# Optimization experiments

Hardware: AMD Instinct MI355X
Metric: run time of the kernel (lower is better)

Reference implementation:

```python
import jax, jax.numpy as jnp
import numpy as np

LEAKY_ALPHA = 0.2
NEG_INF = -9e15


def setup_inputs() -> dict:
    key = jax.random.key(0)
    k1, k2, k3, k4, k5 = jax.random.split(key, 5)
    n, n_head, f_in, f_out = 4096, 8, 1024, 128
    scale_w = float(np.sqrt(6.0 / (f_in + f_out)))      # xavier_uniform over (f_in,f_out)
    scale_a = float(np.sqrt(6.0 / (f_out + 1)))
    return {
        "h": jax.random.normal(k1, (n, f_in), dtype=jnp.float32),
        "adj": jax.random.randint(k2, (n, n), 0, 2, dtype=jnp.int32),
        "w": jax.random.uniform(k3, (n_head, f_in, f_out), jnp.float32, -scale_w, scale_w),
        "bias": jnp.zeros((f_out,), dtype=jnp.float32),
        "a_src": jax.random.uniform(k4, (n_head, f_out, 1), jnp.float32, -scale_a, scale_a),
        "a_dst": jax.random.uniform(k5, (n_head, f_out, 1), jnp.float32, -scale_a, scale_a),
    }


def reference(h, adj, w, bias, a_src, a_dst):
    n = h.shape[0]
    # per-head projection: [h_head, n, f_out]
    h_prime = jnp.einsum('nf,hfo->hno', h, w)
    attn_src = jnp.einsum('hno,hoi->hn', h_prime, a_src)   # [n_head, n]
    attn_dst = jnp.einsum('hno,hoi->hn', h_prime, a_dst)   # [n_head, n]
    # additive score: attn[h,i,j] = src[h,i] + dst[h,j]
    attn = attn_src[:, :, None] + attn_dst[:, None, :]
    attn = jnp.where(attn >= 0, attn, LEAKY_ALPHA * attn)  # leaky_relu
    attn = jnp.where(adj[None] > 0, attn, NEG_INF)
    attn = jax.nn.softmax(attn, axis=-1)                   # [n_head, n, n]
    # dropout layers are identity in eval mode
    output = jnp.einsum('hnm,hmo->hno', attn, h_prime) + bias
    output = jnp.transpose(output, (1, 0, 2)).reshape(n, -1)  # [n, n_head*f_out]
    weight = jnp.sum(attn, axis=0)                          # [n, n]
    return output, weight
```

## Files before the change

kernel.cpp:

```cpp
#include <hip/hip_runtime.h>
#include <hip/hip_bf16.h>


#define N 4096
#define NH 8
#define FIN 1024
#define FOUT 128

typedef short bf16x8 __attribute__((ext_vector_type(8)));
typedef float f32x4 __attribute__((ext_vector_type(4)));
typedef unsigned int uint;
typedef unsigned short ushort;

__device__ __forceinline__ float b2f(ushort u){ return __uint_as_float(((uint)u)<<16); }
__device__ __forceinline__ uint pk2cvt(float a, float b){
    float2 f; f.x=a; f.y=b;
    __hip_bfloat162 h = __float22bfloat162_rn(f);
    uint r; __builtin_memcpy(&r, &h, 4); return r;
}
__device__ __forceinline__ float sane(float x, float lim){ return fminf(fmaxf(x,-lim),lim); }
__device__ __forceinline__ int swz(int r, int cg){ return r*64 + (((cg) ^ (r & 7)) << 3); }
__device__ __forceinline__ void glds16(const ushort* g, ushort* l){
    __builtin_amdgcn_global_load_lds(
        (const __attribute__((address_space(1))) void*)g,
        (__attribute__((address_space(3))) void*)l, 16, 0, 0);
}
__device__ __forceinline__ int detect_mode(const ushort* hraw){
    ushort u = hraw[2*(threadIdx.x & 63)];
    int e = (u>>7)&0xFF;
    unsigned long long m = __ballot(e>=90 && e<=141);
    return (__popcll(m)>=40)?0:1;
}

__global__ __launch_bounds__(256) void prep(
        const int* __restrict__ adj, uint* __restrict__ bitsT,
        float* __restrict__ acc, float* __restrict__ lsum, int nacc,
        const void* __restrict__ wraw, const ushort* __restrict__ hraw,
        ushort* __restrict__ wT) {
    __shared__ ushort tile[64][72];
    int b = blockIdx.x, t = threadIdx.x;
    if (b < 65536) {
        size_t idx = (size_t)b * 256 + t;
        int v = adj[idx];
        unsigned long long m = __ballot(v != 0);
        int lane = t & 63;
        uint i  = (uint)(idx >> 12);
        uint jw = ((uint)idx & 4095u) >> 5;
        if (lane == 0)       bitsT[jw * N + i] = (uint)m;
        else if (lane == 32) bitsT[jw * N + i] = (uint)(m >> 32);
        return;
    }
    int zb = b - 65536;
    if (zb < nacc + 32) {
        float4 z; z.x=0.f; z.y=0.f; z.z=0.f; z.w=0.f;
        if (zb < nacc) reinterpret_cast<float4*>(acc)[(size_t)zb*256+t] = z;
        else           reinterpret_cast<float4*>(lsum)[(size_t)(zb-nacc)*256+t] = z;
        return;
    }
    int bb = zb - (nacc + 32);
    int mode = detect_mode(hraw);
    int f0 = (bb & 15) * 64, o0 = ((bb >> 4) & 1) * 64, h = bb >> 5;
#pragma unroll
    for (int it = 0; it < 2; ++it) {
        int slot = it * 256 + t;
        int row = slot >> 3, c = slot & 7;
        size_t eoff = (size_t)h * (FIN * FOUT) + (size_t)(f0 + row) * FOUT + o0 + c * 8;
        alignas(16) ushort tmp[8];
        if (mode == 0) {
            *reinterpret_cast<uint4*>(tmp) = *reinterpret_cast<const uint4*>((const ushort*)wraw + eoff);
        } else {
            const float* wF = (const float*)wraw;
            float4 x = *reinterpret_cast<const float4*>(wF + eoff);
            float4 y = *reinterpret_cast<const float4*>(wF + eoff + 4);
            uint4 p; p.x = pk2cvt(x.x,x.y); p.y = pk2cvt(x.z,x.w);
            p.z = pk2cvt(y.x,y.y); p.w = pk2cvt(y.z,y.w);
            *reinterpret_cast<uint4*>(tmp) = p;
        }
        *reinterpret_cast<uint4*>(&tile[row][c * 8]) = *reinterpret_cast<uint4*>(tmp);
    }
    __syncthreads();
#pragma unroll
    for (int it = 0; it < 2; ++it) {
        int slot = it * 256 + t;
        int orow = slot >> 3, c = slot & 7;
        alignas(16) ushort tmp[8];
#pragma unroll
        for (int k = 0; k < 8; ++k) tmp[k] = tile[c * 8 + k][orow];
        *reinterpret_cast<uint4*>(wT + (size_t)h * (FIN * FOUT) + (size_t)(o0 + orow) * FIN + f0 + c * 8) =
            *reinterpret_cast<uint4*>(tmp);
    }
}

__global__ __launch_bounds__(256) void gemm_hp(
        const void* __restrict__ hraw, const ushort* __restrict__ wT,
        const void* __restrict__ asraw, const void* __restrict__ adraw,
        ushort* __restrict__ hpT,
        float* __restrict__ es1, float* __restrict__ es2,
        float* __restrict__ ed1, float* __restrict__ ed2) {
    __shared__ ushort Bs[2][FOUT * 64];
    __shared__ float sred[64], dred[64];
    int mode = detect_mode((const ushort*)hraw);
    int t = threadIdx.x;
    int lin = blockIdx.x + 64 * blockIdx.y;
    int i0 = (((lin & 7) * 8) + ((lin >> 6) & 7)) * 64;
    int head = (lin >> 3) & 7;
    int w = t >> 6, lane = t & 63, quad = lane >> 4, l16 = lane & 15, wsh = quad * 8;
    int arow = i0 + w * 16 + l16;
    const ushort* hU = (const ushort*)hraw;
    const float*  hF = (const float*)hraw;
    int l8 = lane >> 3, lk = (lane & 7) ^ (l8 & 7);
    const ushort* gs[4];
#pragma unroll
    for (int s = 0; s < 4; ++s) {
        int o = (w * 4 + s) * 8 + l8;
        gs[s] = wT + (size_t)head * FOUT * FIN + (size_t)o * FIN + lk * 8;
    }

    float asv[8], adv[8];
#pragma unroll
    for (int n = 0; n < 8; ++n) {
        int ai = head * FOUT + n * 16 + l16;
        asv[n] = mode ? ((const float*)asraw)[ai] : b2f(((const ushort*)asraw)[ai]);
        adv[n] = mode ? ((const float*)adraw)[ai] : b2f(((const ushort*)adraw)[ai]);
    }

    f32x4 acc[8] = {};
#pragma unroll
    for (int s = 0; s < 4; ++s) glds16(gs[s], &Bs[0][(w * 4 + s) * 512]);
    uint4 au[2]; float4 af[2][2];
    if (mode == 0) {
#pragma unroll
        for (int kk = 0; kk < 2; ++kk)
            au[kk] = *reinterpret_cast<const uint4*>(hU + (size_t)arow * FIN + kk * 32 + wsh);
    } else {
#pragma unroll
        for (int kk = 0; kk < 2; ++kk) {
            af[kk][0] = *reinterpret_cast<const float4*>(hF + (size_t)arow * FIN + kk * 32 + wsh);
            af[kk][1] = *reinterpret_cast<const float4*>(hF + (size_t)arow * FIN + kk * 32 + wsh + 4);
        }
    }
    __syncthreads();

    for (int c = 0; c < 16; ++c) {
        int k0 = c * 64;
        if (c < 15) {
            ushort* bsw = &Bs[(c + 1) & 1][0];
#pragma unroll
            for (int s = 0; s < 4; ++s)
                glds16(gs[s] + k0 + 64, &bsw[(w * 4 + s) * 512]);
        }
        bf16x8 a2[2];
        if (mode == 0) {
            a2[0] = *reinterpret_cast<bf16x8*>(&au[0]);
            a2[1] = *reinterpret_cast<bf16x8*>(&au[1]);
        } else {
#pragma unroll
            for (int kk = 0; kk < 2; ++kk) {
                uint4 av; av.x = pk2cvt(af[kk][0].x, af[kk][0].y); av.y = pk2cvt(af[kk][0].z, af[kk][0].w);
                av.z = pk2cvt(af[kk][1].x, af[kk][1].y); av.w = pk2cvt(af[kk][1].z, af[kk][1].w);
                a2[kk] = *reinterpret_cast<bf16x8*>(&av);
            }
        }
        if (c < 15) {
            if (mode == 0) {
#pragma unroll
                for (int kk = 0; kk < 2; ++kk)
                    au[kk] = *reinterpret_cast<const uint4*>(hU + (size_t)arow * FIN + k0 + 64 + kk * 32 + wsh);
            } else {
#pragma unroll
                for (int kk = 0; kk < 2; ++kk) {
                    af[kk][0] = *reinterpret_cast<const float4*>(hF + (size_t)arow * FIN + k0 + 64 + kk * 32 + wsh);
                    af[kk][1] = *reinterpret_cast<const float4*>(hF + (size_t)arow * FIN + k0 + 64 + kk * 32 + wsh + 4);
                }
            }
        }
        const ushort* bsr = &Bs[c & 1][0];
#pragma unroll
        for (int kk = 0; kk < 2; ++kk) {
            int cg0 = kk * 4 + quad;
#pragma unroll
            for (int n = 0; n < 8; ++n) {
                bf16x8 b = *reinterpret_cast<const bf16x8*>(&bsr[swz(n * 16 + l16, cg0)]);
                acc[n] = __builtin_amdgcn_mfma_f32_16x16x32_bf16(a2[kk], b, acc[n], 0, 0, 0);
            }
        }
        if (c < 15) __syncthreads();
    }
#pragma unroll
    for (int n = 0; n < 8; ++n) {
        uint2 pk;
        pk.x = pk2cvt(acc[n][0], acc[n][1]);
        pk.y = pk2cvt(acc[n][2], acc[n][3]);
        *reinterpret_cast<uint2*>(hpT + ((size_t)head * FOUT + n * 16 + l16) * N + i0 + w * 16 + quad * 4) = pk;
    }
#pragma unroll
    for (int rr = 0; rr < 4; ++rr) {
        float s = 0.f, d = 0.f;
#pragma unroll
        for (int n = 0; n < 8; ++n) { s += acc[n][rr] * asv[n]; d += acc[n][rr] * adv[n]; }
#pragma unroll
        for (int off = 1; off < 16; off <<= 1) { s += __shfl_xor(s, off); d += __shfl_xor(d, off); }
        if (l16 == 0) { sred[w * 16 + quad * 4 + rr] = s; dred[w * 16 + quad * 4 + rr] = d; }
    }
    __syncthreads();
    if (t < 64) {
        int i = i0 + t;
        float s = sane(sred[t], 30.f);
        float d = sane(dred[t], 30.f);
        es1[head * N + i] = __expf(s);       es2[head * N + i] = __expf(0.2f * s);
        ed1[head * N + i] = __expf(d);       ed2[head * N + i] = __expf(0.2f * d);
    }
}

__global__ __launch_bounds__(256, 4) void pv_kernel(
        const ushort* __restrict__ hpT,
        const float* __restrict__ es1, const float* __restrict__ es2,
        const float* __restrict__ ed1, const float* __restrict__ ed2,
        const uint* __restrict__ bitsT,
        float* __restrict__ accOut, float* __restrict__ lsum, int use_atomic) {
    __shared__ ushort Bs[2][FOUT * 64];
    __shared__ float Ed[2][1024];
    int t = threadIdx.x;
    int lin = blockIdx.x + 32 * blockIdx.y + 256 * blockIdx.z;
    int g  = (lin & 7) * 4 + (lin >> 8);
    int ib = (lin >> 3) & 31;
    int hh = g & 7, kz = g >> 3;
    int i0 = ib * 128, kb = kz * 1024;
    int w = t >> 6, lane = t & 63, quad = lane >> 4, l16 = lane & 15, wsh = quad * 8;
    int irow[2];
    float s1[2], s2[2];
#pragma unroll
    for (int mi = 0; mi < 2; ++mi) {
        irow[mi] = i0 + w * 32 + mi * 16 + l16;
        s1[mi] = es1[hh * N + irow[mi]];
        s2[mi] = es2[hh * N + irow[mi]];
    }
    const uint* bp = bitsT + (size_t)(kb >> 5) * N;
    int l8 = lane >> 3, lk = (lane & 7) ^ (l8 & 7);
    const ushort* gs[4];
#pragma unroll
    for (int s = 0; s < 4; ++s) {
        int o = (w * 4 + s) * 8 + l8;
        gs[s] = hpT + (size_t)hh * FOUT * N + (size_t)o * N + kb + lk * 8;
    }
    bf16x8 ones;
#pragma unroll
    for (int j = 0; j < 8; ++j) ones[j] = (short)0x3F80;

    f32x4 acc[2][8] = {};
    f32x4 accl[2] = {};

    float4 ev1 = *reinterpret_cast<const float4*>(ed1 + hh * N + kb + t * 4);
    float4 ev2 = *reinterpret_cast<const float4*>(ed2 + hh * N + kb + t * 4);
    uint bwc[2][2], bwn[2][2];
#pragma unroll
    for (int kk = 0; kk < 2; ++kk)
#pragma unroll
        for (int mi = 0; mi < 2; ++mi) bwc[kk][mi] = bp[(size_t)kk * N + irow[mi]];
#pragma unroll
    for (int s = 0; s < 4; ++s) glds16(gs[s], &Bs[0][(w * 4 + s) * 512]);
    *reinterpret_cast<float4*>(&Ed[0][t * 4]) = ev1;
    *reinterpret_cast<float4*>(&Ed[1][t * 4]) = ev2;
    __syncthreads();

    for (int c = 0; c < 16; ++c) {
        if (c < 15) {
            ushort* bsw = &Bs[(c + 1) & 1][0];
#pragma unroll
            for (int s = 0; s < 4; ++s)
                glds16(gs[s] + (c + 1) * 64, &bsw[(w * 4 + s) * 512]);
#pragma unroll
            for (int kk = 0; kk < 2; ++kk)
#pragma unroll
                for (int mi = 0; mi < 2; ++mi)
                    bwn[kk][mi] = bp[(size_t)((c + 1) * 2 + kk) * N + irow[mi]];
        }
        const ushort* bsr = &Bs[c & 1][0];
#pragma unroll
        for (int kk = 0; kk < 2; ++kk) {
            int kgl = c * 64 + kk * 32 + wsh;
            float4 d1a = *reinterpret_cast<const float4*>(&Ed[0][kgl]);
            float4 d1b = *reinterpret_cast<const float4*>(&Ed[0][kgl + 4]);
            float4 d2a = *reinterpret_cast<const float4*>(&Ed[1][kgl]);
            float4 d2b = *reinterpret_cast<const float4*>(&Ed[1][kgl + 4]);
            bf16x8 am[2];
#pragma unroll
            for (int mi = 0; mi < 2; ++mi) {
                uint word = bwc[kk][mi] >> wsh;
                float e0 = fmaxf(s1[mi]*d1a.x, s2[mi]*d2a.x); e0 = (word & 1u)   ? e0 : 0.f;
                float e1 = fmaxf(s1[mi]*d1a.y, s2[mi]*d2a.y); e1 = (word & 2u)   ? e1 : 0.f;
                float e2 = fmaxf(s1[mi]*d1a.z, s2[mi]*d2a.z); e2 = (word & 4u)   ? e2 : 0.f;
                float e3 = fmaxf(s1[mi]*d1a.w, s2[mi]*d2a.w); e3 = (word & 8u)   ? e3 : 0.f;
                float e4 = fmaxf(s1[mi]*d1b.x, s2[mi]*d2b.x); e4 = (word & 16u)  ? e4 : 0.f;
                float e5 = fmaxf(s1[mi]*d1b.y, s2[mi]*d2b.y); e5 = (word & 32u)  ? e5 : 0.f;
                float e6 = fmaxf(s1[mi]*d1b.z, s2[mi]*d2b.z); e6 = (word & 64u)  ? e6 : 0.f;
                float e7 = fmaxf(s1[mi]*d1b.w, s2[mi]*d2b.w); e7 = (word & 128u) ? e7 : 0.f;
                uint4 av; av.x = pk2cvt(e0, e1); av.y = pk2cvt(e2, e3);
                av.z = pk2cvt(e4, e5); av.w = pk2cvt(e6, e7);
                am[mi] = *reinterpret_cast<bf16x8*>(&av);
                accl[mi] = __builtin_amdgcn_mfma_f32_16x16x32_bf16(am[mi], ones, accl[mi], 0, 0, 0);
            }
            int cg0 = kk * 4 + quad;
            __builtin_amdgcn_s_setprio(1);
#pragma unroll
            for (int n = 0; n < 8; ++n) {
                bf16x8 b = *reinterpret_cast<const bf16x8*>(&bsr[swz(n * 16 + l16, cg0)]);
                acc[0][n] = __builtin_amdgcn_mfma_f32_16x16x32_bf16(am[0], b, acc[0][n], 0, 0, 0);
                acc[1][n] = __builtin_amdgcn_mfma_f32_16x16x32_bf16(am[1], b, acc[1][n], 0, 0, 0);
            }
            __builtin_amdgcn_s_setprio(0);
        }
#pragma unroll
        for (int kk = 0; kk < 2; ++kk)
#pragma unroll
            for (int mi = 0; mi < 2; ++mi) bwc[kk][mi] = bwn[kk][mi];
        if (c < 15) __syncthreads();
    }
    if (l16 == 0) {
#pragma unroll
        for (int mi = 0; mi < 2; ++mi)
#pragma unroll
            for (int rr = 0; rr < 4; ++rr)
                atomicAdd(&lsum[hh * N + i0 + w * 32 + mi * 16 + quad * 4 + rr], accl[mi][rr]);
    }
    if (use_atomic) {
#pragma unroll
        for (int mi = 0; mi < 2; ++mi) {
            float* arow = accOut + ((size_t)hh * N + i0 + w * 32 + mi * 16 + quad * 4) * FOUT + l16;
#pragma unroll
            for (int n = 0; n < 8; ++n)
#pragma unroll
                for (int rr = 0; rr < 4; ++rr)
                    atomicAdd(&arow[(size_t)rr * FOUT + n * 16], acc[mi][n][rr]);
        }
    } else {
        float* part = accOut + (size_t)kz * ((size_t)NH * N * FOUT);
#pragma unroll
        for (int mi = 0; mi < 2; ++mi) {
            float* arow = part + ((size_t)hh * N + i0 + w * 32 + mi * 16 + quad * 4) * FOUT + l16;
#pragma unroll
            for (int n = 0; n < 8; ++n)
#pragma unroll
                for (int rr = 0; rr < 4; ++rr)
                    arow[(size_t)rr * FOUT + n * 16] = acc[mi][n][rr];
        }
    }
}

__global__ __launch_bounds__(256) void pv_epi(
        const float* __restrict__ acc32, const float* __restrict__ lsum,
        const float* __restrict__ es1, const float* __restrict__ es2,
        const void* __restrict__ braw, const ushort* __restrict__ hraw,
        void* __restrict__ outraw,
        float* __restrict__ s1r, float* __restrict__ s2r, int nparts) {
    int mode = detect_mode(hraw);
    int idx4 = blockIdx.x * 256 + threadIdx.x;
    int h = idx4 >> 17;
    int i = (idx4 >> 5) & 4095;
    int og = idx4 & 31;
    const size_t PSTRIDE4 = (size_t)NH * N * FOUT / 4;
    float4 v = reinterpret_cast<const float4*>(acc32)[idx4];
    if (nparts == 4) {
        float4 a = reinterpret_cast<const float4*>(acc32)[PSTRIDE4 + idx4];
        float4 b = reinterpret_cast<const float4*>(acc32)[2 * PSTRIDE4 + idx4];
        float4 c = reinterpret_cast<const float4*>(acc32)[3 * PSTRIDE4 + idx4];
        v.x += a.x + b.x + c.x; v.y += a.y + b.y + c.y;
        v.z += a.z + b.z + c.z; v.w += a.w + b.w + c.w;
    }
    float lv = lsum[h * N + i];
    float r = (lv > 1e-30f) ? 1.0f / lv : 0.f;
    if (og == 0) {
        s1r[h * N + i] = es1[h * N + i] * r;
        s2r[h * N + i] = es2[h * N + i] * r;
    }
    float4 bv;
    if (mode) bv = reinterpret_cast<const float4*>(braw)[og];
    else {
        const ushort* bu = (const ushort*)braw;
        bv.x = b2f(bu[og*4]); bv.y = b2f(bu[og*4+1]); bv.z = b2f(bu[og*4+2]); bv.w = b2f(bu[og*4+3]);
    }
    v.x = v.x * r + bv.x; v.y = v.y * r + bv.y; v.z = v.z * r + bv.z; v.w = v.w * r + bv.w;
    size_t ob = (size_t)i * (NH * FOUT) + h * FOUT + og * 4;
    if (mode) *reinterpret_cast<float4*>((float*)outraw + ob) = v;
    else {
        uint2 pk; pk.x = pk2cvt(v.x, v.y); pk.y = pk2cvt(v.z, v.w);
        *reinterpret_cast<uint2*>((ushort*)outraw + ob) = pk;
    }
}

__global__ __launch_bounds__(256) void weight_kernel(
        const float* __restrict__ s1r, const float* __restrict__ s2r,
        const float* __restrict__ ed1, const float* __restrict__ ed2,
        const uint* __restrict__ bitsT,
        const ushort* __restrict__ hraw,
        void* __restrict__ outraw) {
    int mode = detect_mode(hraw);
    ushort* woutU = (ushort*)outraw + (size_t)N * (NH * FOUT);
    float*  woutF = (float*)outraw  + (size_t)N * (NH * FOUT);
    int t = threadIdx.x;
    int j = blockIdx.x * 1024 + t * 4;
    int i0 = blockIdx.y * 32;
    float4 d1[NH], d2[NH];
#pragma unroll
    for (int hh = 0; hh < NH; ++hh) {
        d1[hh] = *reinterpret_cast<const float4*>(ed1 + hh * N + j);
        d2[hh] = *reinterpret_cast<const float4*>(ed2 + hh * N + j);
    }
    int wrow = j >> 5;
    int jsh = j & 31;
    for (int i = i0; i < i0 + 32; ++i) {
        uint wbits = bitsT[(size_t)wrow * N + i] >> jsh;
        float sx = 0.f, sy = 0.f, sz = 0.f, sw = 0.f;
#pragma unroll
        for (int hh = 0; hh < NH; ++hh) {
            float a = s1r[hh * N + i];
            float b = s2r[hh * N + i];
            sx += fmaxf(a * d1[hh].x, b * d2[hh].x);
            sy += fmaxf(a * d1[hh].y, b * d2[hh].y);
            sz += fmaxf(a * d1[hh].z, b * d2[hh].z);
            sw += fmaxf(a * d1[hh].w, b * d2[hh].w);
        }
        sx = (wbits & 1u) ? sx : 0.f;
        sy = (wbits & 2u) ? sy : 0.f;
        sz = (wbits & 4u) ? sz : 0.f;
        sw = (wbits & 8u) ? sw : 0.f;
        size_t oidx = (size_t)i * N + j;
        if (mode) {
            float4 st; st.x = sx; st.y = sy; st.z = sz; st.w = sw;
            *reinterpret_cast<float4*>(woutF + oidx) = st;
        } else {
            uint2 pk; pk.x = pk2cvt(sx, sy); pk.y = pk2cvt(sz, sw);
            *reinterpret_cast<uint2*>(woutU + oidx) = pk;
        }
    }
}

extern "C" void kernel_launch(void* const* d_in, const int* in_sizes, int n_in,
                              void* d_out, int out_size, void* d_ws, size_t ws_size,
                              hipStream_t stream) {
    (void)in_sizes; (void)n_in; (void)out_size;
    const void* hraw  = d_in[0];
    const int*  adj   = (const int*)d_in[1];
    const void* wraw  = d_in[2];
    const void* braw  = d_in[3];
    const void* asraw = d_in[4];
    const void* adraw = d_in[5];

    char* ws = (char*)d_ws;
    float* lsum = (float*)(ws + 0);
    float* es1  = (float*)(ws + 262144);
    float* es2  = (float*)(ws + 393216);
    float* ed1  = (float*)(ws + 524288);
    float* ed2  = (float*)(ws + 655360);
    float* s1r  = (float*)(ws + 786432);
    float* s2r  = (float*)(ws + 917504);
    uint*  bitsT= (uint*)(ws + 1048576);
    ushort* wT  = (ushort*)(ws + 3145728);

    const size_t SMALL_END = 5242880;
    const size_t PART = 16777216;
    float*  acc32; ushort* hpT;
    int use_atomic, nparts;
    if (ws_size >= SMALL_END + 4 * PART + 8388608ull) {
        char* b = ws + SMALL_END;
        acc32 = (float*)b;
        hpT   = (ushort*)(b + 4 * PART);
        use_atomic = 0; nparts = 4;
    } else if (ws_size >= SMALL_END + 25165824ull) {
        char* b = ws + SMALL_END;
        acc32 = (float*)b;
        hpT   = (ushort*)(b + PART);
        use_atomic = 1; nparts = 1;
    } else {
        char* ob = (char*)d_out;
        acc32 = (float*)(ob + 16777216);
        hpT   = (ushort*)(ob + 33554432);
        use_atomic = 1; nparts = 1;
    }

    int nacc = use_atomic ? 4096 : 0;
    prep<<<65536 + nacc + 32 + 256, 256, 0, stream>>>(adj, bitsT, acc32, lsum, nacc,
                                                      wraw, (const ushort*)hraw, wT);
    gemm_hp<<<dim3(64, 8), 256, 0, stream>>>(hraw, wT, asraw, adraw, hpT,
                                             es1, es2, ed1, ed2);
    pv_kernel<<<dim3(32, 8, 4), 256, 0, stream>>>(hpT, es1, es2, ed1, ed2, bitsT,
                                                  acc32, lsum, use_atomic);
    pv_epi<<<4096, 256, 0, stream>>>(acc32, lsum, es1, es2, braw, (const ushort*)hraw,
                                     d_out, s1r, s2r, nparts);
    weight_kernel<<<dim3(4, 128), 256, 0, stream>>>(s1r, s2r, ed1, ed2, bitsT,
                                                    (const ushort*)hraw, d_out);
}
```

Before: 285.0 us.

## Merge output epilogue and weight kernel into one launch; simplify gemm block mapping

Fuses the per-head output normalization epilogue and the summed-attention weight kernel into a single launch, with block ranges split between the two roles. The weight path now recomputes the normalized source scores from lsum and es1/es2 instead of reading intermediates written by the epilogue. This removes a launch and a dependency but repeats a division per head per row. It also replaces the swizzled block-to-tile mapping in the projection GEMM with a plain head-major grid, which may change L2 reuse of the shared h rows.

Result: slower. 319.8 us (+12.2%).

```diff
diff --git a/kernel.cpp b/kernel.cpp
--- a/kernel.cpp
+++ b/kernel.cpp
@@ -101,9 +101,8 @@
     __shared__ float sred[64], dred[64];
     int mode = detect_mode((const ushort*)hraw);
     int t = threadIdx.x;
-    int lin = blockIdx.x + 64 * blockIdx.y;
-    int i0 = (((lin & 7) * 8) + ((lin >> 6) & 7)) * 64;
-    int head = (lin >> 3) & 7;
+    int head = blockIdx.x;
+    int i0 = blockIdx.y * 64;
     int w = t >> 6, lane = t & 63, quad = lane >> 4, l16 = lane & 15, wsh = quad * 8;
     int arow = i0 + w * 16 + l16;
     const ushort* hU = (const ushort*)hraw;
@@ -347,59 +346,51 @@
     }
 }
 
-__global__ __launch_bounds__(256) void pv_epi(
+__global__ __launch_bounds__(256) void finale(
         const float* __restrict__ acc32, const float* __restrict__ lsum,
         const float* __restrict__ es1, const float* __restrict__ es2,
-        const void* __restrict__ braw, const ushort* __restrict__ hraw,
-        void* __restrict__ outraw,
-        float* __restrict__ s1r, float* __restrict__ s2r, int nparts) {
-    int mode = detect_mode(hraw);
-    int idx4 = blockIdx.x * 256 + threadIdx.x;
-    int h = idx4 >> 17;
-    int i = (idx4 >> 5) & 4095;
-    int og = idx4 & 31;
-    const size_t PSTRIDE4 = (size_t)NH * N * FOUT / 4;
-    float4 v = reinterpret_cast<const float4*>(acc32)[idx4];
-    if (nparts == 4) {
-        float4 a = reinterpret_cast<const float4*>(acc32)[PSTRIDE4 + idx4];
-        float4 b = reinterpret_cast<const float4*>(acc32)[2 * PSTRIDE4 + idx4];
-        float4 c = reinterpret_cast<const float4*>(acc32)[3 * PSTRIDE4 + idx4];
-        v.x += a.x + b.x + c.x; v.y += a.y + b.y + c.y;
-        v.z += a.z + b.z + c.z; v.w += a.w + b.w + c.w;
-    }
-    float lv = lsum[h * N + i];
-    float r = (lv > 1e-30f) ? 1.0f / lv : 0.f;
-    if (og == 0) {
-        s1r[h * N + i] = es1[h * N + i] * r;
-        s2r[h * N + i] = es2[h * N + i] * r;
-    }
-    float4 bv;
-    if (mode) bv = reinterpret_cast<const float4*>(braw)[og];
-    else {
-        const ushort* bu = (const ushort*)braw;
-        bv.x = b2f(bu[og*4]); bv.y = b2f(bu[og*4+1]); bv.z = b2f(bu[og*4+2]); bv.w = b2f(bu[og*4+3]);
-    }
-    v.x = v.x * r + bv.x; v.y = v.y * r + bv.y; v.z = v.z * r + bv.z; v.w = v.w * r + bv.w;
-    size_t ob = (size_t)i * (NH * FOUT) + h * FOUT + og * 4;
-    if (mode) *reinterpret_cast<float4*>((float*)outraw + ob) = v;
-    else {
-        uint2 pk; pk.x = pk2cvt(v.x, v.y); pk.y = pk2cvt(v.z, v.w);
-        *reinterpret_cast<uint2*>((ushort*)outraw + ob) = pk;
-    }
-}
-
-__global__ __launch_bounds__(256) void weight_kernel(
-        const float* __restrict__ s1r, const float* __restrict__ s2r,
         const float* __restrict__ ed1, const float* __restrict__ ed2,
         const uint* __restrict__ bitsT,
-        const ushort* __restrict__ hraw,
-        void* __restrict__ outraw) {
+        const void* __restrict__ braw, const ushort* __restrict__ hraw,
+        void* __restrict__ outraw, int nparts) {
     int mode = detect_mode(hraw);
+    int b = blockIdx.x, t = threadIdx.x;
+    if (b < 4096) {
+        int idx4 = b * 256 + t;
+        int h = idx4 >> 17;
+        int i = (idx4 >> 5) & 4095;
+        int og = idx4 & 31;
+        const size_t PSTRIDE4 = (size_t)NH * N * FOUT / 4;
+        float4 v = reinterpret_cast<const float4*>(acc32)[idx4];
+        if (nparts == 4) {
+            float4 a = reinterpret_cast<const float4*>(acc32)[PSTRIDE4 + idx4];
+            float4 bq = reinterpret_cast<const float4*>(acc32)[2 * PSTRIDE4 + idx4];
+            float4 c = reinterpret_cast<const float4*>(acc32)[3 * PSTRIDE4 + idx4];
+            v.x += a.x + bq.x + c.x; v.y += a.y + bq.y + c.y;
+            v.z += a.z + bq.z + c.z; v.w += a.w + bq.w + c.w;
+        }
+        float lv = lsum[h * N + i];
+        float r = (lv > 1e-30f) ? 1.0f / lv : 0.f;
+        float4 bv;
+        if (mode) bv = reinterpret_cast<const float4*>(braw)[og];
+        else {
+            const ushort* bu = (const ushort*)braw;
+            bv.x = b2f(bu[og*4]); bv.y = b2f(bu[og*4+1]); bv.z = b2f(bu[og*4+2]); bv.w = b2f(bu[og*4+3]);
+        }
+        v.x = v.x * r + bv.x; v.y = v.y * r + bv.y; v.z = v.z * r + bv.z; v.w = v.w * r + bv.w;
+        size_t ob = (size_t)i * (NH * FOUT) + h * FOUT + og * 4;
+        if (mode) *reinterpret_cast<float4*>((float*)outraw + ob) = v;
+        else {
+            uint2 pk; pk.x = pk2cvt(v.x, v.y); pk.y = pk2cvt(v.z, v.w);
+            *reinterpret_cast<uint2*>((ushort*)outraw + ob) = pk;
+        }
+        return;
+    }
+    int wb = b - 4096;
     ushort* woutU = (ushort*)outraw + (size_t)N * (NH * FOUT);
     float*  woutF = (float*)outraw  + (size_t)N * (NH * FOUT);
-    int t = threadIdx.x;
-    int j = blockIdx.x * 1024 + t * 4;
-    int i0 = blockIdx.y * 32;
+    int j = (wb & 3) * 1024 + t * 4;
+    int i0 = (wb >> 2) * 32;
     float4 d1[NH], d2[NH];
 #pragma unroll
     for (int hh = 0; hh < NH; ++hh) {
@@ -413,12 +404,14 @@
         float sx = 0.f, sy = 0.f, sz = 0.f, sw = 0.f;
 #pragma unroll
         for (int hh = 0; hh < NH; ++hh) {
-            float a = s1r[hh * N + i];
-            float b = s2r[hh * N + i];
-            sx += fmaxf(a * d1[hh].x, b * d2[hh].x);
-            sy += fmaxf(a * d1[hh].y, b * d2[hh].y);
-            sz += fmaxf(a * d1[hh].z, b * d2[hh].z);
-            sw += fmaxf(a * d1[hh].w, b * d2[hh].w);
+            float lv = lsum[hh * N + i];
+            float r = (lv > 1e-30f) ? 1.0f / lv : 0.f;
+            float a = es1[hh * N + i] * r;
+            float bq = es2[hh * N + i] * r;
+            sx += fmaxf(a * d1[hh].x, bq * d2[hh].x);
+            sy += fmaxf(a * d1[hh].y, bq * d2[hh].y);
+            sz += fmaxf(a * d1[hh].z, bq * d2[hh].z);
+            sw += fmaxf(a * d1[hh].w, bq * d2[hh].w);
         }
         sx = (wbits & 1u) ? sx : 0.f;
         sy = (wbits & 2u) ? sy : 0.f;
@@ -452,8 +445,6 @@
     float* es2  = (float*)(ws + 393216);
     float* ed1  = (float*)(ws + 524288);
     float* ed2  = (float*)(ws + 655360);
-    float* s1r  = (float*)(ws + 786432);
-    float* s2r  = (float*)(ws + 917504);
     uint*  bitsT= (uint*)(ws + 1048576);
     ushort* wT  = (ushort*)(ws + 3145728);
 
@@ -481,12 +472,10 @@
     int nacc = use_atomic ? 4096 : 0;
     prep<<<65536 + nacc + 32 + 256, 256, 0, stream>>>(adj, bitsT, acc32, lsum, nacc,
                                                       wraw, (const ushort*)hraw, wT);
-    gemm_hp<<<dim3(64, 8), 256, 0, stream>>>(hraw, wT, asraw, adraw, hpT,
+    gemm_hp<<<dim3(8, 64), 256, 0, stream>>>(hraw, wT, asraw, adraw, hpT,
                                              es1, es2, ed1, ed2);
     pv_kernel<<<dim3(32, 8, 4), 256, 0, stream>>>(hpT, es1, es2, ed1, ed2, bitsT,
                                                   acc32, lsum, use_atomic);
-    pv_epi<<<4096, 256, 0, stream>>>(acc32, lsum, es1, es2, braw, (const ushort*)hraw,
-                                     d_out, s1r, s2r, nparts);
-    weight_kernel<<<dim3(4, 128), 256, 0, stream>>>(s1r, s2r, ed1, ed2, bitsT,
-                                                    (const ushort*)hraw, d_out);
-}
+    finale<<<4608, 256, 0, stream>>>(acc32, lsum, es1, es2, ed1, ed2, bitsT,
+                                     braw, (const ushort*)hraw, d_out, nparts);
+}
```
